# Kernel tuning notes

Measured on AMD Instinct MI355X. Metric: run time of the kernel, lower is better.

Reference implementation:

```python
import jax, jax.numpy as jnp
import numpy as np

B, T, C = 2, 2048, 2048
H, KVH, D = 16, 4, 128
EPS = 1.1920929e-07  # torch.finfo(float32).eps, default for F.rms_norm


def setup_inputs() -> dict:
    key = jax.random.key(0)
    ks = jax.random.split(key, 5)
    x = jax.random.normal(ks[0], (B, T, C), jnp.float32)
    # standard RoPE angle tables, shaped to broadcast over [B, T, heads, D/2]
    half = D // 2
    inv_freq = 1.0 / (10000.0 ** (np.arange(half, dtype=np.float64) / half))
    ang = np.arange(T, dtype=np.float64)[:, None] * inv_freq[None, :]
    cos = jnp.asarray(np.cos(ang), jnp.float32)[None, :, None, :]
    sin = jnp.asarray(np.sin(ang), jnp.float32)[None, :, None, :]
    s = C ** -0.5
    Wq = jax.random.normal(ks[1], (H * D, C), jnp.float32) * s
    Wk = jax.random.normal(ks[2], (KVH * D, C), jnp.float32) * s
    Wv = jax.random.normal(ks[3], (KVH * D, C), jnp.float32) * s
    Wo = jax.random.normal(ks[4], (C, C), jnp.float32) * s
    return {"x": x, "cos": cos, "sin": sin, "Wq": Wq, "Wk": Wk, "Wv": Wv, "Wo": Wo}


def _rope(x, cos, sin):
    d = x.shape[-1] // 2
    x1, x2 = x[..., :d], x[..., d:]
    return jnp.concatenate([x1 * cos + x2 * sin, -x1 * sin + x2 * cos], axis=-1)


def _rmsnorm(x):
    return x * jax.lax.rsqrt(jnp.mean(x * x, axis=-1, keepdims=True) + EPS)


def reference(x, cos, sin, Wq, Wk, Wv, Wo):
    Bx, Tx, Cx = x.shape
    q = (x @ Wq.T).reshape(Bx, Tx, H, D)
    k = (x @ Wk.T).reshape(Bx, Tx, KVH, D)
    v = (x @ Wv.T).reshape(Bx, Tx, KVH, D)
    q = _rmsnorm(_rope(q, cos, sin))
    k = _rmsnorm(_rope(k, cos, sin))
    # [B, heads, T, D]
    q = q.transpose(0, 2, 1, 3)
    k = k.transpose(0, 2, 1, 3)
    v = v.transpose(0, 2, 1, 3)
    groups = H // KVH  # GQA: replicate kv heads
    k = jnp.repeat(k, groups, axis=1)
    v = jnp.repeat(v, groups, axis=1)
    scale = 1.0 / jnp.sqrt(jnp.asarray(D, x.dtype))
    scores = jnp.einsum('bhqd,bhkd->bhqk', q, k) * scale
    causal = jnp.tril(jnp.ones((Tx, Tx), dtype=bool))
    scores = jnp.where(causal, scores, jnp.finfo(scores.dtype).min)
    att = jax.nn.softmax(scores, axis=-1)
    y = jnp.einsum('bhqk,bhkd->bhqd', att, v)
    y = y.transpose(0, 2, 1, 3).reshape(Bx, Tx, H * D)
    return y @ Wo.T
```

## Files before the change

kernel.cpp:

```cpp
#include <hip/hip_runtime.h>
#include <hip/hip_bf16.h>

typedef unsigned short u16t;
typedef unsigned int   u32t;
typedef float  f32x4 __attribute__((ext_vector_type(4)));
typedef short  s16x8 __attribute__((ext_vector_type(8)));
typedef unsigned int u32x4 __attribute__((ext_vector_type(4)));
typedef float  f4 __attribute__((ext_vector_type(4)));

#define BB 2
#define TT 2048
#define CC 2048
#define HH 16
#define KVHN 4
#define DD 128
#define EPSV 1.1920929e-07f
#define SCALE 0.08838834764831845f
#define MFIX 12.0f

__device__ __forceinline__ float b2f(u16t u){ union{u32t i; float f;} x; x.i=((u32t)u)<<16; return x.f; }
__device__ __forceinline__ u16t f2b(float f){ union{float f; u32t i;} x; x.f=f; u32t r = x.i + 0x7fffu + ((x.i>>16)&1u); return (u16t)(r>>16); }
__device__ __forceinline__ u32t pk2(float a, float b){
    __hip_bfloat162 h = __float22bfloat162_rn(make_float2(a,b));
    u32t r; __builtin_memcpy(&r,&h,4); return r;
}
__device__ __forceinline__ s16x8 ldf(const u16t* p){ s16x8 r; __builtin_memcpy(&r,p,16); return r; }
__device__ __forceinline__ void st16(u16t* p, u32x4 v){ __builtin_memcpy(p,&v,16); }
__device__ __forceinline__ u32x4 ldg16(const u16t* p){ u32x4 r; __builtin_memcpy(&r,p,16); return r; }

typedef const __attribute__((address_space(1))) unsigned int ga_u32;
typedef __attribute__((address_space(3))) unsigned int ls_u32;
__device__ __forceinline__ void gl16(const u16t* g, u16t* l) {
    __builtin_amdgcn_global_load_lds((ga_u32*)(unsigned long long)(g),
                                     (ls_u32*)(unsigned int)(unsigned long long)(l),
                                     16, 0, 0);
}

#define BARRIER() __builtin_amdgcn_s_barrier()
#define SCHEDB()  __builtin_amdgcn_sched_barrier(0)
#define WAITLG0() asm volatile("s_waitcnt lgkmcnt(0)" ::: "memory")
#define WAITLG2() asm volatile("s_waitcnt lgkmcnt(2)" ::: "memory")
#define WAITLG4() asm volatile("s_waitcnt lgkmcnt(4)" ::: "memory")
#define WAITLG6() asm volatile("s_waitcnt lgkmcnt(6)" ::: "memory")
#define WAITLG8() asm volatile("s_waitcnt lgkmcnt(8)" ::: "memory")
#define WAITVM8() asm volatile("s_waitcnt vmcnt(8)" ::: "memory")
#define WAITVM6() asm volatile("s_waitcnt vmcnt(6)" ::: "memory")
#define WAITVM4() asm volatile("s_waitcnt vmcnt(4)" ::: "memory")
#define WAITVM0() asm volatile("s_waitcnt vmcnt(0)" ::: "memory")

__global__ __launch_bounds__(256) void cvt_kernel(
    const float* __restrict__ x,  const float* __restrict__ wq,
    const float* __restrict__ wk, const float* __restrict__ wv,
    const float* __restrict__ wo,
    u16t* __restrict__ xb, u16t* __restrict__ wqb, u16t* __restrict__ wkb,
    u16t* __restrict__ wvb, u16t* __restrict__ wob)
{
    size_t g = (size_t)blockIdx.x * 256 + threadIdx.x;
    const float* src; u16t* dst; size_t off;
    if      (g < 1048576) { src = x;  dst = xb;  off = g; }
    else if (g < 1572864) { src = wq; dst = wqb; off = g - 1048576; }
    else if (g < 1703936) { src = wk; dst = wkb; off = g - 1572864; }
    else if (g < 1835008) { src = wv; dst = wvb; off = g - 1703936; }
    else                  { src = wo; dst = wob; off = g - 1835008; }
    f4 a = *(const f4*)(src + off*8);
    f4 b = *(const f4*)(src + off*8 + 4);
    u32x4 o = { pk2(a[0],a[1]), pk2(a[2],a[3]), pk2(b[0],b[1]), pk2(b[2],b[3]) };
    st16(dst + off*8, o);
}

template<int NF>
__device__ __forceinline__ void gemm256(
    const u16t* __restrict__ aPanel, const u16t* __restrict__ bPanel,
    u16t* lds, f32x4 (&acc)[4][NF], const int tid)
{
    constexpr int BQ = NF/2;
    u16t* Abuf[2] = { lds,         lds + 16384 };
    u16t* Bbuf[2] = { lds + 32768, lds + 32768 + NF*2048 };
    const int w = tid>>6, quad = (tid>>4)&3, l15 = tid&15;
    const int wr = (w>>1)*64, wc = (w&1)*(NF*16);
    const int gcol = (((tid&7) ^ ((tid>>3)&7)) << 3);
    const u16t* aB = aPanel + (size_t)(tid>>3)*CC + gcol;
    const u16t* bB = bPanel + (size_t)(tid>>3)*CC + gcol;

    #pragma unroll
    for (int i=0;i<4;++i)
        #pragma unroll
        for (int j=0;j<NF;++j)
            #pragma unroll
            for (int r=0;r<4;++r) acc[i][j][r] = 0.f;

    #pragma unroll
    for (int i=0;i<4;++i)  gl16(aB + (size_t)(i*64)*CC,      Abuf[0] + (i*512+tid)*8);
    #pragma unroll
    for (int i=0;i<BQ;++i) gl16(bB + (size_t)(i*64)*CC,      Bbuf[0] + (i*512+tid)*8);
    SCHEDB();
    #pragma unroll
    for (int i=0;i<4;++i)  gl16(aB + (size_t)(i*64)*CC + 64, Abuf[1] + (i*512+tid)*8);
    #pragma unroll
    for (int i=0;i<BQ;++i) gl16(bB + (size_t)(i*64)*CC + 64, Bbuf[1] + (i*512+tid)*8);

    s16x8 afr[2][4];
    s16x8 bfr[3][BQ];

    #pragma unroll 2
    for (int kt=0; kt<32; ++kt){
        const u16t* Ac = Abuf[kt&1];
        const u16t* Bc = Bbuf[kt&1];
        if (kt == 31) { WAITVM0(); }
        else { if constexpr (NF==8) { WAITVM8(); } else { WAITVM6(); } }
        SCHEDB();
        BARRIER();

        #pragma unroll
        for (int mi=0;mi<4;++mi){
            const int row = wr + mi*16 + l15;
            afr[0][mi] = ldf(Ac + row*64 + ((quad ^ (row&7))<<3));
        }
        #pragma unroll
        for (int ni=0;ni<BQ;++ni){
            const int row = wc + ni*16 + l15;
            bfr[0][ni] = ldf(Bc + row*64 + ((quad ^ (row&7))<<3));
        }
        SCHEDB();
        #pragma unroll
        for (int ni=0;ni<BQ;++ni){
            const int row = wc + BQ*16 + ni*16 + l15;
            bfr[1][ni] = ldf(Bc + row*64 + ((quad ^ (row&7))<<3));
        }
        if constexpr (NF==8) { WAITLG4(); } else { WAITLG2(); }
        SCHEDB();
        __builtin_amdgcn_s_setprio(1);
        #pragma unroll
        for (int mi=0;mi<4;++mi)
            #pragma unroll
            for (int ni=0;ni<BQ;++ni)
                acc[mi][ni] = __builtin_amdgcn_mfma_f32_16x16x32_bf16(
                    afr[0][mi], bfr[0][ni], acc[mi][ni], 0,0,0);
        __builtin_amdgcn_s_setprio(0);
        #pragma unroll
        for (int mi=0;mi<4;++mi){
            const int row = wr + mi*16 + l15;
            afr[1][mi] = ldf(Ac + row*64 + (((4|quad) ^ (row&7))<<3));
        }
        #pragma unroll
        for (int ni=0;ni<BQ;++ni){
            const int row = wc + ni*16 + l15;
            bfr[2][ni] = ldf(Bc + row*64 + (((4|quad) ^ (row&7))<<3));
        }
        if constexpr (NF==8) { WAITLG8(); } else { WAITLG6(); }
        SCHEDB();
        __builtin_amdgcn_s_setprio(1);
        #pragma unroll
        for (int mi=0;mi<4;++mi)
            #pragma unroll
            for (int ni=0;ni<BQ;++ni)
                acc[mi][BQ+ni] = __builtin_amdgcn_mfma_f32_16x16x32_bf16(
                    afr[0][mi], bfr[1][ni], acc[mi][BQ+ni], 0,0,0);
        __builtin_amdgcn_s_setprio(0);
        #pragma unroll
        for (int ni=0;ni<BQ;++ni){
            const int row = wc + BQ*16 + ni*16 + l15;
            bfr[0][ni] = ldf(Bc + row*64 + (((4|quad) ^ (row&7))<<3));
        }
        if constexpr (NF==8) { WAITLG4(); } else { WAITLG2(); }
        SCHEDB();
        __builtin_amdgcn_s_setprio(1);
        #pragma unroll
        for (int mi=0;mi<4;++mi)
            #pragma unroll
            for (int ni=0;ni<BQ;++ni)
                acc[mi][ni] = __builtin_amdgcn_mfma_f32_16x16x32_bf16(
                    afr[1][mi], bfr[2][ni], acc[mi][ni], 0,0,0);
        __builtin_amdgcn_s_setprio(0);
        WAITLG0();
        SCHEDB();
        __builtin_amdgcn_s_setprio(1);
        #pragma unroll
        for (int mi=0;mi<4;++mi)
            #pragma unroll
            for (int ni=0;ni<BQ;++ni)
                acc[mi][BQ+ni] = __builtin_amdgcn_mfma_f32_16x16x32_bf16(
                    afr[1][mi], bfr[0][ni], acc[mi][BQ+ni], 0,0,0);
        __builtin_amdgcn_s_setprio(0);

        BARRIER();
        if (kt < 30){
            const int k0 = (kt+2)*64;
            u16t* Ad = Abuf[kt&1]; u16t* Bd = Bbuf[kt&1];
            #pragma unroll
            for (int i=0;i<4;++i)  gl16(aB + (size_t)(i*64)*CC + k0, Ad + (i*512+tid)*8);
            #pragma unroll
            for (int i=0;i<BQ;++i) gl16(bB + (size_t)(i*64)*CC + k0, Bd + (i*512+tid)*8);
        }
    }
}

__global__ __launch_bounds__(512,2) void qkv_kernel(
    const u16t* __restrict__ xb, const u16t* __restrict__ wqb,
    const u16t* __restrict__ wkb, const u16t* __restrict__ wvb,
    const float* __restrict__ cosp, const float* __restrict__ sinp,
    u16t* __restrict__ qws, u16t* __restrict__ kws, u16t* __restrict__ vtw)
{
    __shared__ __align__(16) u16t lds[65536];
    const int tid = threadIdx.x;
    const int bx = blockIdx.x, by = blockIdx.y;
    const int m0 = bx*256;

    int type, headbase; const u16t* W;
    if (by < 8)       { type=0; W = wqb + (size_t)by*256*CC;      headbase = by*2; }
    else if (by < 10) { type=1; W = wkb + (size_t)(by-8)*256*CC;  headbase = (by-8)*2; }
    else              { type=2; W = wvb + (size_t)(by-10)*256*CC; headbase = (by-10)*2; }

    f32x4 acc[4][8];
    gemm256<8>(xb + (size_t)m0*CC, W, lds, acc, tid);

    const int w = tid>>6, quad = (tid>>4)&3, l15 = tid&15;
    const int wr = (w>>1)*64, wn = w&1;
    const int head = headbase + wn;
    const int bb = bx>>3;
    const int ttb = (m0 + wr) & 2047;

    if (type == 2){
        u16t* vb = vtw + (size_t)(bb*KVHN+head)*DD*TT;
        #pragma unroll
        for (int mi=0;mi<4;++mi){
            const int tt = ttb + mi*16 + quad*4;
            #pragma unroll
            for (int ni=0;ni<8;++ni){
                const int d = ni*16 + l15;
                u16t o[4];
                #pragma unroll
                for (int r=0;r<4;++r) o[r] = f2b(acc[mi][ni][r]);
                __builtin_memcpy(vb + (size_t)d*TT + tt, o, 8);
            }
        }
    } else {
        u16t* dst = (type==0) ? (qws + (size_t)(bb*HH+head)*TT*DD)
                              : (kws + (size_t)(bb*KVHN+head)*TT*DD);
        #pragma unroll
        for (int mi=0;mi<4;++mi){
            const int tt0 = ttb + mi*16 + quad*4;
            float ss[4] = {0.f,0.f,0.f,0.f};
            #pragma unroll
            for (int ni=0;ni<8;++ni)
                #pragma unroll
                for (int r=0;r<4;++r) ss[r] += acc[mi][ni][r]*acc[mi][ni][r];
            float rms[4];
            #pragma unroll
            for (int r=0;r<4;++r){
                float s = ss[r];
                s += __shfl_xor(s, 1, 16);
                s += __shfl_xor(s, 2, 16);
                s += __shfl_xor(s, 4, 16);
                s += __shfl_xor(s, 8, 16);
                rms[r] = rsqrtf(s*(1.f/128.f) + EPSV);
            }
            #pragma unroll
            for (int ni=0;ni<4;++ni){
                const int j = ni*16 + l15;
                #pragma unroll
                for (int r=0;r<4;++r){
                    const int tt = tt0 + r;
                    const float c = cosp[tt*64 + j];
                    const float s = sinp[tt*64 + j];
                    const float z1 = acc[mi][ni][r], z2 = acc[mi][ni+4][r];
                    dst[(size_t)tt*DD + j]      = f2b((z1*c + z2*s)*rms[r]);
                    dst[(size_t)tt*DD + j + 64] = f2b((z2*c - z1*s)*rms[r]);
                }
            }
        }
    }
}

__global__ __launch_bounds__(512,2) void attn_kernel(
    const u16t* __restrict__ qws, const u16t* __restrict__ kws,
    const u16t* __restrict__ vtw, u16t* __restrict__ yws)
{
    __shared__ __align__(16) u16t lds[49152];
    u16t* Ps = lds + 32768;

    const int tid = threadIdx.x;
    const int w = tid>>6, lane = tid&63, quad = lane>>4, l15 = lane&15;
    const int bx = blockIdx.x, h = blockIdx.y, b = blockIdx.z, kvh = h>>2;

    const int qti    = (w < 4) ? (15 - bx) : bx;
    const int qwbase = qti*128 + (w&3)*32;
    const int nkt    = (16 - bx)*2;

    const u16t* kb = kws + (size_t)(b*KVHN+kvh)*TT*DD;
    const u16t* vb = vtw + (size_t)(b*KVHN+kvh)*DD*TT;

    const int krow = tid>>4;
    const int kcg  = (tid&15) ^ ((tid>>4)&7);
    const int vrow = tid>>3;
    const int vcg  = (tid&7)  ^ ((tid>>3)&7);

    const u16t* qp = qws + ((size_t)(b*HH+h)*TT + qwbase + l15)*DD + quad*8;
    s16x8 qf[2][4];
    #pragma unroll
    for (int mi=0;mi<2;++mi)
        #pragma unroll
        for (int kq=0;kq<4;++kq)
            qf[mi][kq] = ldf(qp + (size_t)mi*16*DD + kq*32);

    {
        u16t* Kd = lds;        u16t* Vd = lds + 16384;
        gl16(kb + (size_t)(krow)*DD + kcg*8,        Kd + tid*8);
        gl16(kb + (size_t)(krow+32)*DD + kcg*8,     Kd + (512+tid)*8);
        gl16(vb + (size_t)(vrow)*TT + vcg*8,        Vd + tid*8);
        gl16(vb + (size_t)(vrow+64)*TT + vcg*8,     Vd + (512+tid)*8);
        SCHEDB();
        Kd = lds + 8192;       Vd = lds + 24576;
        gl16(kb + (size_t)(krow+64)*DD + kcg*8,      Kd + tid*8);
        gl16(kb + (size_t)(krow+96)*DD + kcg*8,      Kd + (512+tid)*8);
        gl16(vb + (size_t)(vrow)*TT + 64 + vcg*8,    Vd + tid*8);
        gl16(vb + (size_t)(vrow+64)*TT + 64 + vcg*8, Vd + (512+tid)*8);
    }

    f32x4 o_[2][8];
    float l_[2][4];
    #pragma unroll
    for (int mi=0;mi<2;++mi){
        #pragma unroll
        for (int r=0;r<4;++r) l_[mi][r] = 0.f;
        #pragma unroll
        for (int n8=0;n8<8;++n8)
            #pragma unroll
            for (int r=0;r<4;++r) o_[mi][n8][r] = 0.f;
    }

    const int swz = (l15&7)<<3;

    for (int kt=0; kt<nkt; ++kt){
        const int k0 = kt*64;
        if (kt+1 == nkt) { WAITVM0(); } else { WAITVM4(); }
        SCHEDB();
        BARRIER();
        if (k0 <= qwbase + 31) {
            const u16t* Ks = (kt&1) ? (lds + 8192)  : lds;
            const u16t* Vt = (kt&1) ? (lds + 24576) : (lds + 16384);

            f32x4 s[2][4];
            #pragma unroll
            for (int mi=0;mi<2;++mi)
                #pragma unroll
                for (int ni=0;ni<4;++ni)
                    #pragma unroll
                    for (int r=0;r<4;++r) s[mi][ni][r] = 0.f;
            #pragma unroll
            for (int kq=0;kq<4;++kq){
                s16x8 kf[4];
                #pragma unroll
                for (int ni=0;ni<4;++ni)
                    kf[ni] = ldf(Ks + (ni*16+l15)*128 + (((kq*4+quad)<<3) ^ swz));
                __builtin_amdgcn_s_setprio(1);
                #pragma unroll
                for (int mi=0;mi<2;++mi)
                    #pragma unroll
                    for (int ni=0;ni<4;++ni)
                        s[mi][ni] = __builtin_amdgcn_mfma_f32_16x16x32_bf16(qf[mi][kq], kf[ni], s[mi][ni], 0,0,0);
                __builtin_amdgcn_s_setprio(0);
            }

            const bool need_mask = (k0 + 63) > qwbase;
            #pragma unroll
            for (int mi=0;mi<2;++mi){
                const int qrow = qwbase + mi*16 + quad*4;
                #pragma unroll
                for (int ni=0;ni<4;++ni){
                    const int kcol = k0 + ni*16 + l15;
                    #pragma unroll
                    for (int r=0;r<4;++r){
                        float p = __expf(__builtin_fmaf(s[mi][ni][r], SCALE, -MFIX));
                        if (need_mask && kcol > qrow + r) p = 0.f;
                        l_[mi][r] += p;
                        const int rw = w*32 + mi*16 + quad*4 + r;
                        Ps[rw*64 + ((ni*16+l15) ^ (((quad*4+r)&7)<<3))] = f2b(p);
                    }
                }
            }

            #pragma unroll
            for (int ks=0;ks<2;++ks){
                s16x8 pf[2];
                #pragma unroll
                for (int mi=0;mi<2;++mi)
                    pf[mi] = ldf(Ps + (w*32+mi*16+l15)*64 + (((ks*4+quad)<<3) ^ swz));
                __builtin_amdgcn_s_setprio(1);
                #pragma unroll
                for (int n8=0;n8<8;++n8){
                    s16x8 vf = ldf(Vt + (n8*16+l15)*64 + (((ks*4+quad)<<3) ^ swz));
                    #pragma unroll
                    for (int mi=0;mi<2;++mi)
                        o_[mi][n8] = __builtin_amdgcn_mfma_f32_16x16x32_bf16(pf[mi], vf, o_[mi][n8], 0,0,0);
                }
                __builtin_amdgcn_s_setprio(0);
            }
        }
        BARRIER();
        if (kt+2 < nkt){
            const int kn = (kt+2)*64;
            u16t* Kd = (kt&1) ? (lds + 8192)  : lds;
            u16t* Vd = (kt&1) ? (lds + 24576) : (lds + 16384);
            gl16(kb + (size_t)(kn+krow)*DD + kcg*8,      Kd + tid*8);
            gl16(kb + (size_t)(kn+krow+32)*DD + kcg*8,   Kd + (512+tid)*8);
            gl16(vb + (size_t)(vrow)*TT + kn + vcg*8,    Vd + tid*8);
            gl16(vb + (size_t)(vrow+64)*TT + kn + vcg*8, Vd + (512+tid)*8);
        }
    }

    #pragma unroll
    for (int mi=0;mi<2;++mi){
        const int qrow = qwbase + mi*16 + quad*4;
        float inv[4];
        #pragma unroll
        for (int r=0;r<4;++r){
            float lt = l_[mi][r];
            lt += __shfl_xor(lt,1,16);
            lt += __shfl_xor(lt,2,16);
            lt += __shfl_xor(lt,4,16);
            lt += __shfl_xor(lt,8,16);
            inv[r] = 1.f/lt;
        }
        #pragma unroll
        for (int n8=0;n8<8;++n8)
            #pragma unroll
            for (int r=0;r<4;++r)
                yws[((size_t)(b*TT + qrow + r))*2048 + h*DD + n8*16 + l15] = f2b(o_[mi][n8][r]*inv[r]);
    }
}

__global__ __launch_bounds__(512,2) void oproj_kernel(
    const u16t* __restrict__ y, const u16t* __restrict__ wob, float* __restrict__ out)
{
    __shared__ __align__(16) u16t lds[49152];
    const int tid = threadIdx.x;
    const int m0 = blockIdx.x*256, n0 = blockIdx.y*128;

    f32x4 acc[4][4];
    gemm256<4>(y + (size_t)m0*CC, wob + (size_t)n0*CC, lds, acc, tid);

    const int w = tid>>6, quad = (tid>>4)&3, l15 = tid&15;
    const int wr = (w>>1)*64, wc = (w&1)*64;
    #pragma unroll
    for (int mi=0;mi<4;++mi){
        const int m = m0 + wr + mi*16 + quad*4;
        #pragma unroll
        for (int ni=0;ni<4;++ni){
            const int n = n0 + wc + ni*16 + l15;
            #pragma unroll
            for (int r=0;r<4;++r)
                out[(size_t)(m+r)*CC + n] = acc[mi][ni][r];
        }
    }
}

extern "C" void kernel_launch(void* const* d_in, const int* in_sizes, int n_in,
                              void* d_out, int out_size, void* d_ws, size_t ws_size,
                              hipStream_t stream) {
    const float* x    = (const float*)d_in[0];
    const float* cosp = (const float*)d_in[1];
    const float* sinp = (const float*)d_in[2];
    const float* Wq   = (const float*)d_in[3];
    const float* Wk   = (const float*)d_in[4];
    const float* Wv   = (const float*)d_in[5];
    const float* Wo   = (const float*)d_in[6];

    u16t* ws  = (u16t*)d_ws;
    u16t* xb  = ws;
    u16t* wqb = xb  + 8388608;
    u16t* wkb = wqb + 4194304;
    u16t* wvb = wkb + 1048576;
    u16t* wob = wvb + 1048576;
    u16t* qws = wob + 4194304;
    u16t* kws = qws + 8388608;
    u16t* vtw = kws + 2097152;
    u16t* yws = xb;
    float* out = (float*)d_out;

    cvt_kernel<<<dim3(9216), 256, 0, stream>>>(x, Wq, Wk, Wv, Wo, xb, wqb, wkb, wvb, wob);
    qkv_kernel<<<dim3(16, 12), 512, 0, stream>>>(xb, wqb, wkb, wvb, cosp, sinp, qws, kws, vtw);
    attn_kernel<<<dim3(8, 16, 2), 512, 0, stream>>>(qws, kws, vtw, yws);
    oproj_kernel<<<dim3(16, 16), 512, 0, stream>>>(yws, wob, out);
}
```

Before: 355.5 us.

## Restructure GEMM main loop into four-phase schedule with finer-grained staggered prefetch

The shared bf16 GEMM loop is reorganized into four MFMA phases, each covering one half of B in one k-half. Each warp's B columns are now split across the two halves of the B tile, with a row-slot swap in the QKV kernel so each head's data stays in one warp. Global-to-LDS prefetches for the next stages are issued in slices between phases instead of in one batch at the end, and the vmcnt waits are adjusted to match. This is meant to overlap memory traffic with compute and cut register pressure from fragment buffers, at the cost of extra barriers per iteration and more complex index mapping in the epilogues.

```diff
diff --git a/kernel.cpp b/kernel.cpp
--- a/kernel.cpp
+++ b/kernel.cpp
@@ -39,12 +39,9 @@
 #define BARRIER() __builtin_amdgcn_s_barrier()
 #define SCHEDB()  __builtin_amdgcn_sched_barrier(0)
 #define WAITLG0() asm volatile("s_waitcnt lgkmcnt(0)" ::: "memory")
-#define WAITLG2() asm volatile("s_waitcnt lgkmcnt(2)" ::: "memory")
 #define WAITLG4() asm volatile("s_waitcnt lgkmcnt(4)" ::: "memory")
-#define WAITLG6() asm volatile("s_waitcnt lgkmcnt(6)" ::: "memory")
-#define WAITLG8() asm volatile("s_waitcnt lgkmcnt(8)" ::: "memory")
-#define WAITVM8() asm volatile("s_waitcnt vmcnt(8)" ::: "memory")
 #define WAITVM6() asm volatile("s_waitcnt vmcnt(6)" ::: "memory")
+#define WAITVM5() asm volatile("s_waitcnt vmcnt(5)" ::: "memory")
 #define WAITVM4() asm volatile("s_waitcnt vmcnt(4)" ::: "memory")
 #define WAITVM0() asm volatile("s_waitcnt vmcnt(0)" ::: "memory")
 
@@ -68,19 +65,20 @@
     st16(dst + off*8, o);
 }
 
-template<int NF>
+template<int NF, bool BSW>
 __device__ __forceinline__ void gemm256(
     const u16t* __restrict__ aPanel, const u16t* __restrict__ bPanel,
     u16t* lds, f32x4 (&acc)[4][NF], const int tid)
 {
     constexpr int BQ = NF/2;
+    constexpr int BS = NF/4;
     u16t* Abuf[2] = { lds,         lds + 16384 };
     u16t* Bbuf[2] = { lds + 32768, lds + 32768 + NF*2048 };
     const int w = tid>>6, quad = (tid>>4)&3, l15 = tid&15;
-    const int wr = (w>>1)*64, wc = (w&1)*(NF*16);
+    const int wr = (w>>1)*64, wc = (w&1)*(BQ*16);
     const int gcol = (((tid&7) ^ ((tid>>3)&7)) << 3);
-    const u16t* aB = aPanel + (size_t)(tid>>3)*CC + gcol;
-    const u16t* bB = bPanel + (size_t)(tid>>3)*CC + gcol;
+    const u16t* aB  = aPanel + (size_t)(tid>>3)*CC + gcol;
+    const u16t* bBr = bPanel + (size_t)(tid>>3)*CC + gcol;
 
     #pragma unroll
     for (int i=0;i<4;++i)
@@ -90,44 +88,53 @@
             for (int r=0;r<4;++r) acc[i][j][r] = 0.f;
 
     #pragma unroll
-    for (int i=0;i<4;++i)  gl16(aB + (size_t)(i*64)*CC,      Abuf[0] + (i*512+tid)*8);
-    #pragma unroll
-    for (int i=0;i<BQ;++i) gl16(bB + (size_t)(i*64)*CC,      Bbuf[0] + (i*512+tid)*8);
+    for (int i=0;i<4;++i) gl16(aB + (size_t)(i*64)*CC, Abuf[0] + (i*512+tid)*8);
+    #pragma unroll
+    for (int s=0;s<2*BS;++s){
+        const int ss = BSW ? ((s==1)?2:((s==2)?1:s)) : s;
+        gl16(bBr + (size_t)(ss*64)*CC, Bbuf[0] + (s*512+tid)*8);
+    }
     SCHEDB();
     #pragma unroll
-    for (int i=0;i<4;++i)  gl16(aB + (size_t)(i*64)*CC + 64, Abuf[1] + (i*512+tid)*8);
-    #pragma unroll
-    for (int i=0;i<BQ;++i) gl16(bB + (size_t)(i*64)*CC + 64, Bbuf[1] + (i*512+tid)*8);
-
-    s16x8 afr[2][4];
-    s16x8 bfr[3][BQ];
+    for (int i=0;i<4;++i) gl16(aB + (size_t)(i*64)*CC + 64, Abuf[1] + (i*512+tid)*8);
+    #pragma unroll
+    for (int s=0;s<BS;++s){
+        const int ss = BSW ? ((s==1)?2:s) : s;
+        gl16(bBr + (size_t)(ss*64)*CC + 64, Bbuf[1] + (s*512+tid)*8);
+    }
+
+    s16x8 af0[4], af1[4], bf[BQ];
 
     #pragma unroll 2
     for (int kt=0; kt<32; ++kt){
         const u16t* Ac = Abuf[kt&1];
         const u16t* Bc = Bbuf[kt&1];
+        u16t* An = Abuf[kt&1];
+        u16t* Bn = Bbuf[kt&1];
+        u16t* Bo = Bbuf[(kt+1)&1];
         if (kt == 31) { WAITVM0(); }
-        else { if constexpr (NF==8) { WAITVM8(); } else { WAITVM6(); } }
+        else { if constexpr (NF==8) { WAITVM6(); } else { WAITVM5(); } }
         SCHEDB();
         BARRIER();
 
         #pragma unroll
         for (int mi=0;mi<4;++mi){
             const int row = wr + mi*16 + l15;
-            afr[0][mi] = ldf(Ac + row*64 + ((quad ^ (row&7))<<3));
+            af0[mi] = ldf(Ac + row*64 + ((quad ^ (row&7))<<3));
         }
         #pragma unroll
         for (int ni=0;ni<BQ;++ni){
             const int row = wc + ni*16 + l15;
-            bfr[0][ni] = ldf(Bc + row*64 + ((quad ^ (row&7))<<3));
-        }
-        SCHEDB();
-        #pragma unroll
-        for (int ni=0;ni<BQ;++ni){
-            const int row = wc + BQ*16 + ni*16 + l15;
-            bfr[1][ni] = ldf(Bc + row*64 + ((quad ^ (row&7))<<3));
-        }
-        if constexpr (NF==8) { WAITLG4(); } else { WAITLG2(); }
+            bf[ni] = ldf(Bc + row*64 + ((quad ^ (row&7))<<3));
+        }
+        #pragma unroll
+        for (int mi=0;mi<4;++mi){
+            const int row = wr + mi*16 + l15;
+            af1[mi] = ldf(Ac + row*64 + (((4|quad) ^ (row&7))<<3));
+        }
+        SCHEDB();
+        BARRIER();
+        WAITLG4();
         SCHEDB();
         __builtin_amdgcn_s_setprio(1);
         #pragma unroll
@@ -135,19 +142,48 @@
             #pragma unroll
             for (int ni=0;ni<BQ;++ni)
                 acc[mi][ni] = __builtin_amdgcn_mfma_f32_16x16x32_bf16(
-                    afr[0][mi], bfr[0][ni], acc[mi][ni], 0,0,0);
+                    af0[mi], bf[ni], acc[mi][ni], 0,0,0);
         __builtin_amdgcn_s_setprio(0);
-        #pragma unroll
-        for (int mi=0;mi<4;++mi){
-            const int row = wr + mi*16 + l15;
-            afr[1][mi] = ldf(Ac + row*64 + (((4|quad) ^ (row&7))<<3));
-        }
+
         #pragma unroll
         for (int ni=0;ni<BQ;++ni){
             const int row = wc + ni*16 + l15;
-            bfr[2][ni] = ldf(Bc + row*64 + (((4|quad) ^ (row&7))<<3));
-        }
-        if constexpr (NF==8) { WAITLG8(); } else { WAITLG6(); }
+            bf[ni] = ldf(Bc + row*64 + (((4|quad) ^ (row&7))<<3));
+        }
+        if (kt < 31){
+            #pragma unroll
+            for (int s=0;s<BS;++s){
+                const int sl = BS + s;
+                const int ss = BSW ? ((sl==2)?1:sl) : sl;
+                gl16(bBr + (size_t)(ss*64)*CC + (kt+1)*64, Bo + (sl*512+tid)*8);
+            }
+        }
+        SCHEDB();
+        BARRIER();
+        WAITLG0();
+        SCHEDB();
+        __builtin_amdgcn_s_setprio(1);
+        #pragma unroll
+        for (int mi=0;mi<4;++mi)
+            #pragma unroll
+            for (int ni=0;ni<BQ;++ni)
+                acc[mi][ni] = __builtin_amdgcn_mfma_f32_16x16x32_bf16(
+                    af1[mi], bf[ni], acc[mi][ni], 0,0,0);
+        __builtin_amdgcn_s_setprio(0);
+
+        #pragma unroll
+        for (int ni=0;ni<BQ;++ni){
+            const int row = NF*16 + wc + ni*16 + l15;
+            bf[ni] = ldf(Bc + row*64 + ((quad ^ (row&7))<<3));
+        }
+        if (kt < 30){
+            #pragma unroll
+            for (int i=0;i<4;++i)
+                gl16(aB + (size_t)(i*64)*CC + (kt+2)*64, An + (i*512+tid)*8);
+        }
+        SCHEDB();
+        BARRIER();
+        WAITLG0();
         SCHEDB();
         __builtin_amdgcn_s_setprio(1);
         #pragma unroll
@@ -155,23 +191,23 @@
             #pragma unroll
             for (int ni=0;ni<BQ;++ni)
                 acc[mi][BQ+ni] = __builtin_amdgcn_mfma_f32_16x16x32_bf16(
-                    afr[0][mi], bfr[1][ni], acc[mi][BQ+ni], 0,0,0);
+                    af0[mi], bf[ni], acc[mi][BQ+ni], 0,0,0);
         __builtin_amdgcn_s_setprio(0);
+
         #pragma unroll
         for (int ni=0;ni<BQ;++ni){
-            const int row = wc + BQ*16 + ni*16 + l15;
-            bfr[0][ni] = ldf(Bc + row*64 + (((4|quad) ^ (row&7))<<3));
-        }
-        if constexpr (NF==8) { WAITLG4(); } else { WAITLG2(); }
-        SCHEDB();
-        __builtin_amdgcn_s_setprio(1);
-        #pragma unroll
-        for (int mi=0;mi<4;++mi)
-            #pragma unroll
-            for (int ni=0;ni<BQ;++ni)
-                acc[mi][ni] = __builtin_amdgcn_mfma_f32_16x16x32_bf16(
-                    afr[1][mi], bfr[2][ni], acc[mi][ni], 0,0,0);
-        __builtin_amdgcn_s_setprio(0);
+            const int row = NF*16 + wc + ni*16 + l15;
+            bf[ni] = ldf(Bc + row*64 + (((4|quad) ^ (row&7))<<3));
+        }
+        if (kt < 30){
+            #pragma unroll
+            for (int s=0;s<BS;++s){
+                const int ss = BSW ? ((s==1)?2:s) : s;
+                gl16(bBr + (size_t)(ss*64)*CC + (kt+2)*64, Bn + (s*512+tid)*8);
+            }
+        }
+        SCHEDB();
+        BARRIER();
         WAITLG0();
         SCHEDB();
         __builtin_amdgcn_s_setprio(1);
@@ -180,18 +216,8 @@
             #pragma unroll
             for (int ni=0;ni<BQ;++ni)
                 acc[mi][BQ+ni] = __builtin_amdgcn_mfma_f32_16x16x32_bf16(
-                    afr[1][mi], bfr[0][ni], acc[mi][BQ+ni], 0,0,0);
+                    af1[mi], bf[ni], acc[mi][BQ+ni], 0,0,0);
         __builtin_amdgcn_s_setprio(0);
-
-        BARRIER();
-        if (kt < 30){
-            const int k0 = (kt+2)*64;
-            u16t* Ad = Abuf[kt&1]; u16t* Bd = Bbuf[kt&1];
-            #pragma unroll
-            for (int i=0;i<4;++i)  gl16(aB + (size_t)(i*64)*CC + k0, Ad + (i*512+tid)*8);
-            #pragma unroll
-            for (int i=0;i<BQ;++i) gl16(bB + (size_t)(i*64)*CC + k0, Bd + (i*512+tid)*8);
-        }
     }
 }
 
@@ -212,7 +238,7 @@
     else              { type=2; W = wvb + (size_t)(by-10)*256*CC; headbase = (by-10)*2; }
 
     f32x4 acc[4][8];
-    gemm256<8>(xb + (size_t)m0*CC, W, lds, acc, tid);
+    gemm256<8,true>(xb + (size_t)m0*CC, W, lds, acc, tid);
 
     const int w = tid>>6, quad = (tid>>4)&3, l15 = tid&15;
     const int wr = (w>>1)*64, wn = w&1;
@@ -227,7 +253,7 @@
             const int tt = ttb + mi*16 + quad*4;
             #pragma unroll
             for (int ni=0;ni<8;++ni){
-                const int d = ni*16 + l15;
+                const int d = ((ni>>2)*64) + ((ni&3)*16) + l15;
                 u16t o[4];
                 #pragma unroll
                 for (int r=0;r<4;++r) o[r] = f2b(acc[mi][ni][r]);
@@ -438,16 +464,16 @@
     const int m0 = blockIdx.x*256, n0 = blockIdx.y*128;
 
     f32x4 acc[4][4];
-    gemm256<4>(y + (size_t)m0*CC, wob + (size_t)n0*CC, lds, acc, tid);
+    gemm256<4,false>(y + (size_t)m0*CC, wob + (size_t)n0*CC, lds, acc, tid);
 
     const int w = tid>>6, quad = (tid>>4)&3, l15 = tid&15;
-    const int wr = (w>>1)*64, wc = (w&1)*64;
+    const int wr = (w>>1)*64, wcq = (w&1)*32;
     #pragma unroll
     for (int mi=0;mi<4;++mi){
         const int m = m0 + wr + mi*16 + quad*4;
         #pragma unroll
         for (int ni=0;ni<4;++ni){
-            const int n = n0 + wc + ni*16 + l15;
+            const int n = n0 + ((ni>>1)*64) + wcq + ((ni&1)*16) + l15;
             #pragma unroll
             for (int r=0;r<4;++r)
                 out[(size_t)(m+r)*CC + n] = acc[mi][ni][r];
```

After: 302.6 us. 1.17x faster.
